# Kernel optimization log

Hardware: AMD Instinct MI355X
Metric: run time of the kernel (lower is better)

Reference implementation:

```python
import jax, jax.numpy as jnp
import numpy as np

B, F, C, NS, P, N = 256, 2048, 16384, 65536, 8, 32
T, W_BU, W_H, P_MARGIN, N_MARGIN = 1.0, 1.0, 10.0, 0.1, 0.1


def setup_inputs() -> dict:
    key = jax.random.key(0)
    ks = jax.random.split(key, 8)
    inputs = jax.random.normal(ks[0], (B, F), jnp.float32)
    targets = jax.random.randint(ks[1], (B,), 0, C)
    # batch global indices: unique (original .item() assumes a single match)
    indexs = jax.random.permutation(ks[2], NS)[:B].astype(jnp.int64) if False else jax.random.permutation(ks[2], jnp.arange(NS))[:B]
    # positive candidates drawn from in-batch indices so they are found in `indexs`
    pos_sel = jax.random.randint(ks[3], (B, P), 0, B)
    ppairs = indexs[pos_sel]
    # negative candidates: arbitrary global indices (mostly not in batch)
    npairs = jax.random.randint(ks[4], (B, N), 0, NS)
    all_label_to_clusterid = jax.random.randint(ks[5], (NS,), 0, C)
    V = jax.random.normal(ks[6], (C, F), jnp.float32)
    V = V / jnp.linalg.norm(V, axis=1, keepdims=True)  # bank rows are L2-normalized by the update rule
    return {"inputs": inputs, "targets": targets, "ppairs": ppairs, "npairs": npairs,
            "indexs": indexs, "all_label_to_clusterid": all_label_to_clusterid, "V": V, "epoch": 1}


def _forward(inputs, targets, ppairs, npairs, indexs, all_label_to_clusterid, V, epoch):
    # Exclusive branch: logits against the memory bank (V treated as constant)
    outputs = (inputs @ V.T) * T  # [B, C]
    logp = jax.nn.log_softmax(outputs, axis=1)
    bu_loss = -jnp.mean(jnp.take_along_axis(logp, targets[:, None], axis=1))

    # ms_loss (use_prior=True, use_table=True)
    ni = inputs / jnp.linalg.norm(inputs, axis=1, keepdims=True)
    sims = ni @ ni.T          # [B, B]
    tsims = ni @ V.T          # [B, C]

    # positives found in the batch: (ppair == indexs).nonzero()
    mp = ppairs[:, :, None] == indexs[None, None, :]        # [B, P, B]
    found_p = jnp.any(mp, axis=2)
    idx_p = jnp.argmax(mp, axis=2)
    psim_b = jnp.take_along_axis(sims, idx_p, axis=1)       # [B, P]
    mask_pb = found_p & (ppairs >= 0)
    # table positive: tsims[i, target] appended if nonzero
    tp = jnp.take_along_axis(tsims, targets[:, None], axis=1)  # [B, 1]
    mask_tp = tp != 0
    psims = jnp.concatenate([psim_b, tp], axis=1)           # [B, P+1]
    pmask = jnp.concatenate([mask_pb, mask_tp], axis=1)

    # negatives found in the batch
    mn = npairs[:, :, None] == indexs[None, None, :]        # [B, N, B]
    found_n = jnp.any(mn, axis=2)
    idx_n = jnp.argmax(mn, axis=2)
    nsim_b = jnp.take_along_axis(sims, idx_n, axis=1)       # [B, N]
    mask_nb = found_n & (npairs >= 0)
    # table negative appended for EVERY npair (indent level in original): tsims[i, clusterid[npair]]
    ncid = all_label_to_clusterid[jnp.clip(npairs, 0, None)]
    tn = jnp.take_along_axis(tsims, ncid, axis=1)           # [B, N]
    mask_tn = (npairs >= 0) & (tn != 0)
    nsims = jnp.concatenate([nsim_b, tn], axis=1)           # [B, 2N]
    nmask = jnp.concatenate([mask_nb, mask_tn], axis=1)

    # thresholds: max(nsims) or -3 (+p_margin); min(psims) or 3 (-n_margin)
    p_thrd = jnp.where(jnp.any(nmask, 1), jnp.max(jnp.where(nmask, nsims, -jnp.inf), 1), -3.0) + P_MARGIN
    n_thrd = jnp.where(jnp.any(pmask, 1), jnp.min(jnp.where(pmask, psims, jnp.inf), 1), 3.0) - N_MARGIN

    hp = pmask & (psims < p_thrd[:, None])
    hn = nmask & (nsims > n_thrd[:, None]) & (nsims < 0.999999)

    hp_sum = jnp.sum(jnp.where(hp, jnp.exp(-2.0 * (psims - 0.5)), 0.0))
    hn_sum = jnp.sum(jnp.where(hn, jnp.exp(50.0 * (nsims - 0.5)), 0.0))
    hp_loss = jnp.where(jnp.any(hp), 0.5 * jnp.log1p(hp_sum), 0.0)
    hn_loss = jnp.where(jnp.any(hn), (1.0 / 50.0) * jnp.log1p(hn_sum), 0.0)
    # original builds hpsims/hnsims with torch.tensor(...), which DETACHES them
    h_loss = jax.lax.stop_gradient(hp_loss + hn_loss)

    loss = W_BU * bu_loss + W_H * h_loss
    return loss, outputs


def reference(inputs, targets, ppairs, npairs, indexs, all_label_to_clusterid, V, epoch):
    return _forward(inputs, targets, ppairs, npairs, indexs, all_label_to_clusterid, V, epoch)
```

## Files before the change

### kernel.cpp

```cpp
#include <hip/hip_runtime.h>
#include <hip/hip_bf16.h>
#include <math.h>

#define B_SZ 256
#define F_SZ 2048
#define C_SZ 16384
#define P_SZ 8
#define N_SZ 32
#define NTILE 256

typedef __bf16 bf16x8 __attribute__((ext_vector_type(8)));
typedef float f32x4 __attribute__((ext_vector_type(4)));
typedef unsigned short us8 __attribute__((ext_vector_type(8)));

typedef __attribute__((address_space(3))) unsigned int lds_u32;
typedef __attribute__((address_space(1))) const unsigned int glb_u32;

#define WAITCNT_VM4   0x0F74
#define WAITCNT_VM0   0x0F70
#define WAITCNT_LGKM0 0xC07F

__device__ __forceinline__ unsigned short f2bf(float x) {
    union { float f; unsigned int u; } v; v.f = x;
    unsigned int r = v.u + 0x7FFFu + ((v.u >> 16) & 1u);
    return (unsigned short)(r >> 16);
}

__global__ __launch_bounds__(256) void prep_kernel(const float* __restrict__ inputs,
                                                   unsigned short* __restrict__ Abf,
                                                   float* __restrict__ norms) {
    const int row = blockIdx.x;
    const int tid = threadIdx.x;
    const float* rp = inputs + (size_t)row * F_SZ + tid * 8;
    float4 v0 = *(const float4*)(rp);
    float4 v1 = *(const float4*)(rp + 4);
    us8 o;
    o[0]=f2bf(v0.x); o[1]=f2bf(v0.y); o[2]=f2bf(v0.z); o[3]=f2bf(v0.w);
    o[4]=f2bf(v1.x); o[5]=f2bf(v1.y); o[6]=f2bf(v1.z); o[7]=f2bf(v1.w);
    *(us8*)(Abf + (size_t)row * F_SZ + tid * 8) = o;
    float ss = v0.x*v0.x + v0.y*v0.y + v0.z*v0.z + v0.w*v0.w
             + v1.x*v1.x + v1.y*v1.y + v1.z*v1.z + v1.w*v1.w;
    __shared__ float red[256];
    red[tid] = ss; __syncthreads();
    for (int s = 128; s > 0; s >>= 1) { if (tid < s) red[tid] += red[tid+s]; __syncthreads(); }
    if (tid == 0) norms[row] = sqrtf(red[0]);
}

#define BM 128
#define BN 64
#define BK 64
#define BPAD 72
#define KITERS (F_SZ / BK)

__global__ __launch_bounds__(256, 2) void gemm_kernel(const unsigned short* __restrict__ Abf,
                                                      const float* __restrict__ V,
                                                      float* __restrict__ Cout,
                                                      float* __restrict__ pmax,
                                                      float* __restrict__ psum) {
    __shared__ unsigned short As[3][BM * BK];
    __shared__ unsigned short Bs[2][BN * BPAD];
    __shared__ float sm[BM * 2], ss2[BM * 2];

    const int tid = threadIdx.x;
    const int lane = tid & 63;
    const int wid = tid >> 6;
    const int wm = wid >> 1, wn = wid & 1;
    const int q = lane >> 4, l16 = lane & 15;

    const int bid = blockIdx.x;
    const int mhalf = (bid >> 3) & 1;
    const int slab  = (bid & 7) | ((bid >> 4) << 3);
    const int bm0 = mhalf * BM;
    const int bn0 = slab * BN;

    f32x4 acc[4][2];
    #pragma unroll
    for (int i = 0; i < 4; i++)
        #pragma unroll
        for (int j = 0; j < 2; j++) acc[i][j] = (f32x4){0.f, 0.f, 0.f, 0.f};

    const int arow = tid >> 3;
    const int akc = (tid & 7) ^ (arow & 7);
    const unsigned short* AgBase = Abf + (size_t)(bm0 + arow) * F_SZ + akc * 8;

    const int bcol = tid >> 2, bseg = tid & 3;
    const float* BgBase = V + (size_t)(bn0 + bcol) * F_SZ + bseg * 16;
    const int bsoff = bcol * BPAD + bseg * 16;

    float4 b0, b1, b2, b3;

    auto issueA = [&](int ring, int k0) {
        #pragma unroll
        for (int j = 0; j < 4; ++j) {
            __builtin_amdgcn_global_load_lds(
                (glb_u32*)(AgBase + (size_t)j * 32 * F_SZ + k0),
                (lds_u32*)&As[ring][(j * 256 + wid * 64) * 8],
                16, 0, 0);
        }
    };
    auto loadB = [&](int k0) {
        b0 = *(const float4*)(BgBase + k0);
        b1 = *(const float4*)(BgBase + k0 + 4);
        b2 = *(const float4*)(BgBase + k0 + 8);
        b3 = *(const float4*)(BgBase + k0 + 12);
    };
    auto writeB = [&](int buf) {
        us8 w0, w1;
        w0[0]=f2bf(b0.x); w0[1]=f2bf(b0.y); w0[2]=f2bf(b0.z); w0[3]=f2bf(b0.w);
        w0[4]=f2bf(b1.x); w0[5]=f2bf(b1.y); w0[6]=f2bf(b1.z); w0[7]=f2bf(b1.w);
        w1[0]=f2bf(b2.x); w1[1]=f2bf(b2.y); w1[2]=f2bf(b2.z); w1[3]=f2bf(b2.w);
        w1[4]=f2bf(b3.x); w1[5]=f2bf(b3.y); w1[6]=f2bf(b3.z); w1[7]=f2bf(b3.w);
        *(us8*)&Bs[buf][bsoff] = w0;
        *(us8*)&Bs[buf][bsoff + 8] = w1;
    };
    auto compute = [&](int ring, int buf) {
        #pragma unroll
        for (int ks = 0; ks < 2; ++ks) {
            bf16x8 af[4], bfv[2];
            const int kc = ks * 4 + q;
            #pragma unroll
            for (int mi = 0; mi < 4; ++mi) {
                const int row = wm * 64 + mi * 16 + l16;
                af[mi] = *(const bf16x8*)&As[ring][row * 64 + (kc ^ (row & 7)) * 8];
            }
            #pragma unroll
            for (int ni = 0; ni < 2; ++ni) {
                const int col = wn * 32 + ni * 16 + l16;
                bfv[ni] = *(const bf16x8*)&Bs[buf][col * BPAD + ks * 32 + q * 8];
            }
            #pragma unroll
            for (int mi = 0; mi < 4; ++mi)
                #pragma unroll
                for (int ni = 0; ni < 2; ++ni)
                    acc[mi][ni] = __builtin_amdgcn_mfma_f32_16x16x32_bf16(af[mi], bfv[ni], acc[mi][ni], 0, 0, 0);
        }
    };

    issueA(0, 0);
    issueA(1, BK);
    loadB(0);
    __builtin_amdgcn_s_waitcnt(WAITCNT_VM0);
    writeB(0);
    __syncthreads();

    int cur = 0;
    int nxt2 = 2;
    #pragma unroll 1
    for (int it = 0; it < KITERS; ++it) {
        if (it + 1 < KITERS) loadB((it + 1) * BK);
        if (it + 2 < KITERS) issueA(nxt2, (it + 2) * BK);
        compute(cur, it & 1);
        if (it + 2 < KITERS)      __builtin_amdgcn_s_waitcnt(WAITCNT_VM4);
        else if (it + 1 < KITERS) __builtin_amdgcn_s_waitcnt(WAITCNT_VM0);
        if (it + 1 < KITERS) {
            writeB((it + 1) & 1);
            __builtin_amdgcn_s_waitcnt(WAITCNT_LGKM0);
            __builtin_amdgcn_s_barrier();
        }
        cur  = (cur == 2) ? 0 : cur + 1;
        nxt2 = (nxt2 == 2) ? 0 : nxt2 + 1;
    }

    #pragma unroll
    for (int mi = 0; mi < 4; ++mi) {
        const int r0 = bm0 + wm * 64 + mi * 16 + q * 4;
        #pragma unroll
        for (int ni = 0; ni < 2; ++ni) {
            const int c0 = bn0 + wn * 32 + ni * 16 + l16;
            #pragma unroll
            for (int r = 0; r < 4; ++r)
                Cout[(size_t)(r0 + r) * C_SZ + c0] = acc[mi][ni][r];
        }
    }

    #pragma unroll
    for (int mi = 0; mi < 4; ++mi) {
        #pragma unroll
        for (int r = 0; r < 4; ++r) {
            float mloc = fmaxf(acc[mi][0][r], acc[mi][1][r]);
            #pragma unroll
            for (int off = 1; off < 16; off <<= 1)
                mloc = fmaxf(mloc, __shfl_xor(mloc, off, 64));
            float sloc = __expf(acc[mi][0][r] - mloc) + __expf(acc[mi][1][r] - mloc);
            #pragma unroll
            for (int off = 1; off < 16; off <<= 1)
                sloc += __shfl_xor(sloc, off, 64);
            if (l16 == 0) {
                const int lrow = wm * 64 + mi * 16 + q * 4 + r;
                sm[lrow * 2 + wn] = mloc;
                ss2[lrow * 2 + wn] = sloc;
            }
        }
    }
    __syncthreads();
    if (tid < BM) {
        float m1 = sm[tid * 2], s1 = ss2[tid * 2];
        float m2 = sm[tid * 2 + 1], s2 = ss2[tid * 2 + 1];
        float nm = fmaxf(m1, m2);
        float s = s1 * __expf(m1 - nm) + s2 * __expf(m2 - nm);
        pmax[(bm0 + tid) * NTILE + slab] = nm;
        psum[(bm0 + tid) * NTILE + slab] = s;
    }
}

__global__ __launch_bounds__(256) void softmax_combine_kernel(
    const float* __restrict__ pmax, const float* __restrict__ psum,
    const float* __restrict__ outputs, const int* __restrict__ targets,
    float* __restrict__ bu_part)
{
    const int row = blockIdx.x;
    const int tid = threadIdx.x;
    __shared__ float rm[256], rs[256];
    rm[tid] = pmax[row * NTILE + tid];
    rs[tid] = psum[row * NTILE + tid];
    __syncthreads();
    for (int s = 128; s > 0; s >>= 1) {
        if (tid < s) {
            float a = rm[tid], sa = rs[tid];
            float b = rm[tid + s], sb = rs[tid + s];
            float nn = fmaxf(a, b);
            rs[tid] = sa * __expf(a - nn) + sb * __expf(b - nn);
            rm[tid] = nn;
        }
        __syncthreads();
    }
    if (tid == 0) {
        float logZ = rm[0] + logf(rs[0]);
        bu_part[row] = -(outputs[(size_t)row * C_SZ + targets[row]] - logZ);
    }
}

__global__ __launch_bounds__(256) void pairs_kernel(
    const float* __restrict__ inputs, const int* __restrict__ targets,
    const int* __restrict__ ppairs, const int* __restrict__ npairs,
    const int* __restrict__ indexs, const int* __restrict__ cluster,
    const float* __restrict__ outputs, const float* __restrict__ norms,
    float* __restrict__ hp_part, float* __restrict__ hn_part,
    int* __restrict__ flag_part)
{
    const int i = blockIdx.x;
    const int tid = threadIdx.x;
    __shared__ int idxbuf[B_SZ];
    __shared__ int pj[P_SZ];
    __shared__ int nj[N_SZ];
    __shared__ float simp[P_SZ];
    __shared__ float simn[N_SZ];
    __shared__ float tnv[N_SZ];
    __shared__ float s_tp;

    idxbuf[tid] = indexs[tid];
    __syncthreads();

    const float* row = outputs + (size_t)i * C_SZ;
    const float ni_norm = norms[i];

    if (tid < P_SZ) {
        int pp = ppairs[i * P_SZ + tid];
        int f = -1;
        if (pp >= 0) for (int j = 0; j < B_SZ; j++) if (idxbuf[j] == pp) { f = j; break; }
        pj[tid] = f;
    } else if (tid < P_SZ + N_SZ) {
        int t = tid - P_SZ;
        int np = npairs[i * N_SZ + t];
        int f = -1;
        if (np >= 0) for (int j = 0; j < B_SZ; j++) if (idxbuf[j] == np) { f = j; break; }
        nj[t] = f;
        int cid = cluster[np < 0 ? 0 : np];
        tnv[t] = row[cid] / ni_norm;
    }
    if (tid == P_SZ + N_SZ) s_tp = row[targets[i]] / ni_norm;
    __syncthreads();

    const int lane = tid & 63, wv = tid >> 6;
    for (int qq = wv; qq < P_SZ + N_SZ; qq += 4) {
        int j = (qq < P_SZ) ? pj[qq] : nj[qq - P_SZ];
        float s = 0.f;
        if (j >= 0) {
            const float* xi = inputs + (size_t)i * F_SZ;
            const float* xj = inputs + (size_t)j * F_SZ;
            float d = 0.f;
            for (int k = lane; k < F_SZ; k += 64) d += xi[k] * xj[k];
            for (int off = 32; off > 0; off >>= 1) d += __shfl_down(d, off);
            s = d / (ni_norm * norms[j]);
        }
        if (lane == 0) { if (qq < P_SZ) simp[qq] = s; else simn[qq - P_SZ] = s; }
    }
    __syncthreads();

    if (tid == 0) {
        float psims[P_SZ + 1]; bool pmask[P_SZ + 1];
        for (int p = 0; p < P_SZ; p++) {
            int pp = ppairs[i * P_SZ + p];
            pmask[p] = (pj[p] >= 0) && (pp >= 0);
            psims[p] = simp[p];
        }
        psims[P_SZ] = s_tp; pmask[P_SZ] = (s_tp != 0.0f);

        float nsims[2 * N_SZ]; bool nmask[2 * N_SZ];
        for (int t = 0; t < N_SZ; t++) {
            int np = npairs[i * N_SZ + t];
            nmask[t] = (nj[t] >= 0) && (np >= 0);
            nsims[t] = simn[t];
            nsims[N_SZ + t] = tnv[t];
            nmask[N_SZ + t] = (np >= 0) && (tnv[t] != 0.0f);
        }
        bool anyp = false, anyn = false;
        float maxn = -INFINITY, minp = INFINITY;
        for (int t = 0; t < 2 * N_SZ; t++) if (nmask[t]) { anyn = true; maxn = fmaxf(maxn, nsims[t]); }
        for (int p = 0; p < P_SZ + 1; p++) if (pmask[p]) { anyp = true; minp = fminf(minp, psims[p]); }
        float p_thrd = (anyn ? maxn : -3.0f) + 0.1f;
        float n_thrd = (anyp ? minp : 3.0f) - 0.1f;
        float hps = 0.f, hns = 0.f; int fl = 0;
        for (int p = 0; p < P_SZ + 1; p++)
            if (pmask[p] && psims[p] < p_thrd) { fl |= 1; hps += expf(-2.0f * (psims[p] - 0.5f)); }
        for (int t = 0; t < 2 * N_SZ; t++)
            if (nmask[t] && nsims[t] > n_thrd && nsims[t] < 0.999999f) { fl |= 2; hns += expf(50.0f * (nsims[t] - 0.5f)); }
        hp_part[i] = hps; hn_part[i] = hns; flag_part[i] = fl;
    }
}

__global__ __launch_bounds__(256) void finalize_kernel(
    const float* __restrict__ bu_part, const float* __restrict__ hp_part,
    const float* __restrict__ hn_part, const int* __restrict__ flag_part,
    float* __restrict__ d_out)
{
    __shared__ float r1[256], r2[256], r3[256];
    __shared__ int rf[256];
    const int tid = threadIdx.x;
    r1[tid] = bu_part[tid]; r2[tid] = hp_part[tid]; r3[tid] = hn_part[tid]; rf[tid] = flag_part[tid];
    __syncthreads();
    for (int s = 128; s > 0; s >>= 1) {
        if (tid < s) { r1[tid] += r1[tid+s]; r2[tid] += r2[tid+s]; r3[tid] += r3[tid+s]; rf[tid] |= rf[tid+s]; }
        __syncthreads();
    }
    if (tid == 0) {
        float bu = r1[0] / (float)B_SZ;
        float hp_loss = (rf[0] & 1) ? 0.5f * log1pf(r2[0]) : 0.0f;
        float hn_loss = (rf[0] & 2) ? (1.0f / 50.0f) * log1pf(r3[0]) : 0.0f;
        d_out[0] = 1.0f * bu + 10.0f * (hp_loss + hn_loss);
    }
}

extern "C" void kernel_launch(void* const* d_in, const int* in_sizes, int n_in,
                              void* d_out, int out_size, void* d_ws, size_t ws_size,
                              hipStream_t stream) {
    const float* inputs  = (const float*)d_in[0];
    const int*   targets = (const int*)d_in[1];
    const int*   ppairs  = (const int*)d_in[2];
    const int*   npairs  = (const int*)d_in[3];
    const int*   indexs  = (const int*)d_in[4];
    const int*   cluster = (const int*)d_in[5];
    const float* V       = (const float*)d_in[6];
    float* out = (float*)d_out;

    char* ws = (char*)d_ws;
    unsigned short* Abf = (unsigned short*)ws;
    float* norms   = (float*)(ws + (size_t)B_SZ * F_SZ * 2);
    float* bu_part = norms + B_SZ;
    float* hp_part = bu_part + B_SZ;
    float* hn_part = hp_part + B_SZ;
    int*   flag_part = (int*)(hn_part + B_SZ);
    float* pmax = (float*)(flag_part + B_SZ);
    float* psum = pmax + (size_t)B_SZ * NTILE;

    prep_kernel<<<B_SZ, 256, 0, stream>>>(inputs, Abf, norms);
    gemm_kernel<<<512, 256, 0, stream>>>(Abf, V, out + 1, pmax, psum);
    softmax_combine_kernel<<<B_SZ, 256, 0, stream>>>(pmax, psum, out + 1, targets, bu_part);
    pairs_kernel<<<B_SZ, 256, 0, stream>>>(inputs, targets, ppairs, npairs, indexs,
                                           cluster, out + 1, norms,
                                           hp_part, hn_part, flag_part);
    finalize_kernel<<<1, 256, 0, stream>>>(bu_part, hp_part, hn_part, flag_part, out);
}
```

Baseline: 300.6 us.

## Deepen B prefetch to two stages, pack bf16 via perm, fuse softmax combine into pairs

The GEMM main loop is unrolled by two and uses two register sets for the fp32 V tiles, so each B tile is loaded two iterations ahead, and the vmcnt wait is relaxed to allow eight loads in flight. The bf16 conversion now packs pairs with a byte-permute instead of per-element round-to-nearest-even, which is cheaper but rounds ties away from zero rather than to even. The separate softmax-combine kernel is merged into the pairs kernel, removing one launch. The extra registers may reduce occupancy.

Result: no change. 301.9 us (+0.4%).

```diff
diff --git a/kernel.cpp b/kernel.cpp
--- a/kernel.cpp
+++ b/kernel.cpp
@@ -16,7 +16,7 @@
 typedef __attribute__((address_space(3))) unsigned int lds_u32;
 typedef __attribute__((address_space(1))) const unsigned int glb_u32;
 
-#define WAITCNT_VM4   0x0F74
+#define WAITCNT_VM8   0x0F78
 #define WAITCNT_VM0   0x0F70
 #define WAITCNT_LGKM0 0xC07F
 
@@ -24,6 +24,11 @@
     union { float f; unsigned int u; } v; v.f = x;
     unsigned int r = v.u + 0x7FFFu + ((v.u >> 16) & 1u);
     return (unsigned short)(r >> 16);
+}
+
+__device__ __forceinline__ unsigned int pk2bf(float x, float y) {
+    union { float f; unsigned int u; } a, b; a.f = x; b.f = y;
+    return __builtin_amdgcn_perm(b.u + 0x8000u, a.u + 0x8000u, 0x07060302u);
 }
 
 __global__ __launch_bounds__(256) void prep_kernel(const float* __restrict__ inputs,
@@ -87,7 +92,8 @@
     const float* BgBase = V + (size_t)(bn0 + bcol) * F_SZ + bseg * 16;
     const int bsoff = bcol * BPAD + bseg * 16;
 
-    float4 b0, b1, b2, b3;
+    float4 a0, a1, a2, a3;
+    float4 c0, c1, c2, c3;
 
     auto issueA = [&](int ring, int k0) {
         #pragma unroll
@@ -98,20 +104,20 @@
                 16, 0, 0);
         }
     };
-    auto loadB = [&](int k0) {
-        b0 = *(const float4*)(BgBase + k0);
-        b1 = *(const float4*)(BgBase + k0 + 4);
-        b2 = *(const float4*)(BgBase + k0 + 8);
-        b3 = *(const float4*)(BgBase + k0 + 12);
-    };
-    auto writeB = [&](int buf) {
-        us8 w0, w1;
-        w0[0]=f2bf(b0.x); w0[1]=f2bf(b0.y); w0[2]=f2bf(b0.z); w0[3]=f2bf(b0.w);
-        w0[4]=f2bf(b1.x); w0[5]=f2bf(b1.y); w0[6]=f2bf(b1.z); w0[7]=f2bf(b1.w);
-        w1[0]=f2bf(b2.x); w1[1]=f2bf(b2.y); w1[2]=f2bf(b2.z); w1[3]=f2bf(b2.w);
-        w1[4]=f2bf(b3.x); w1[5]=f2bf(b3.y); w1[6]=f2bf(b3.z); w1[7]=f2bf(b3.w);
-        *(us8*)&Bs[buf][bsoff] = w0;
-        *(us8*)&Bs[buf][bsoff + 8] = w1;
+    auto loadB0 = [&](int k0) {
+        a0 = *(const float4*)(BgBase + k0);     a1 = *(const float4*)(BgBase + k0 + 4);
+        a2 = *(const float4*)(BgBase + k0 + 8); a3 = *(const float4*)(BgBase + k0 + 12);
+    };
+    auto loadB1 = [&](int k0) {
+        c0 = *(const float4*)(BgBase + k0);     c1 = *(const float4*)(BgBase + k0 + 4);
+        c2 = *(const float4*)(BgBase + k0 + 8); c3 = *(const float4*)(BgBase + k0 + 12);
+    };
+    auto writeB = [&](int buf, int set) {
+        float4 x0 = set ? c0 : a0, x1 = set ? c1 : a1, x2 = set ? c2 : a2, x3 = set ? c3 : a3;
+        uint4 w0 = { pk2bf(x0.x, x0.y), pk2bf(x0.z, x0.w), pk2bf(x1.x, x1.y), pk2bf(x1.z, x1.w) };
+        uint4 w1 = { pk2bf(x2.x, x2.y), pk2bf(x2.z, x2.w), pk2bf(x3.x, x3.y), pk2bf(x3.z, x3.w) };
+        *(uint4*)&Bs[buf][bsoff] = w0;
+        *(uint4*)&Bs[buf][bsoff + 8] = w1;
     };
     auto compute = [&](int ring, int buf) {
         #pragma unroll
@@ -138,27 +144,40 @@
 
     issueA(0, 0);
     issueA(1, BK);
-    loadB(0);
+    loadB0(0);
     __builtin_amdgcn_s_waitcnt(WAITCNT_VM0);
-    writeB(0);
+    writeB(0, 0);
+    loadB1(BK);
     __syncthreads();
 
     int cur = 0;
-    int nxt2 = 2;
     #pragma unroll 1
-    for (int it = 0; it < KITERS; ++it) {
-        if (it + 1 < KITERS) loadB((it + 1) * BK);
-        if (it + 2 < KITERS) issueA(nxt2, (it + 2) * BK);
-        compute(cur, it & 1);
-        if (it + 2 < KITERS)      __builtin_amdgcn_s_waitcnt(WAITCNT_VM4);
-        else if (it + 1 < KITERS) __builtin_amdgcn_s_waitcnt(WAITCNT_VM0);
-        if (it + 1 < KITERS) {
-            writeB((it + 1) & 1);
-            __builtin_amdgcn_s_waitcnt(WAITCNT_LGKM0);
-            __builtin_amdgcn_s_barrier();
-        }
-        cur  = (cur == 2) ? 0 : cur + 1;
-        nxt2 = (nxt2 == 2) ? 0 : nxt2 + 1;
+    for (int it2 = 0; it2 < KITERS; it2 += 2) {
+        {
+            const int it = it2;
+            if (it + 2 < KITERS) { loadB0((it + 2) * BK); issueA((cur + 2) % 3, (it + 2) * BK); }
+            compute(cur, 0);
+            if (it + 2 < KITERS)      __builtin_amdgcn_s_waitcnt(WAITCNT_VM8);
+            else if (it + 1 < KITERS) __builtin_amdgcn_s_waitcnt(WAITCNT_VM0);
+            if (it + 1 < KITERS) {
+                writeB(1, 1);
+                __builtin_amdgcn_s_waitcnt(WAITCNT_LGKM0);
+                __builtin_amdgcn_s_barrier();
+            }
+        }
+        {
+            const int it = it2 + 1;
+            if (it + 2 < KITERS) { loadB1((it + 2) * BK); issueA(cur, (it + 2) * BK); }
+            compute((cur + 1) % 3, 1);
+            if (it + 2 < KITERS)      __builtin_amdgcn_s_waitcnt(WAITCNT_VM8);
+            else if (it + 1 < KITERS) __builtin_amdgcn_s_waitcnt(WAITCNT_VM0);
+            if (it + 1 < KITERS) {
+                writeB(0, 0);
+                __builtin_amdgcn_s_waitcnt(WAITCNT_LGKM0);
+                __builtin_amdgcn_s_barrier();
+            }
+        }
+        cur = (cur + 2) % 3;
     }
 
     #pragma unroll
@@ -166,10 +185,10 @@
         const int r0 = bm0 + wm * 64 + mi * 16 + q * 4;
         #pragma unroll
         for (int ni = 0; ni < 2; ++ni) {
-            const int c0 = bn0 + wn * 32 + ni * 16 + l16;
+            const int c0g = bn0 + wn * 32 + ni * 16 + l16;
             #pragma unroll
             for (int r = 0; r < 4; ++r)
-                Cout[(size_t)(r0 + r) * C_SZ + c0] = acc[mi][ni][r];
+                Cout[(size_t)(r0 + r) * C_SZ + c0g] = acc[mi][ni][r];
         }
     }
 
@@ -203,40 +222,14 @@
     }
 }
 
-__global__ __launch_bounds__(256) void softmax_combine_kernel(
-    const float* __restrict__ pmax, const float* __restrict__ psum,
-    const float* __restrict__ outputs, const int* __restrict__ targets,
-    float* __restrict__ bu_part)
-{
-    const int row = blockIdx.x;
-    const int tid = threadIdx.x;
-    __shared__ float rm[256], rs[256];
-    rm[tid] = pmax[row * NTILE + tid];
-    rs[tid] = psum[row * NTILE + tid];
-    __syncthreads();
-    for (int s = 128; s > 0; s >>= 1) {
-        if (tid < s) {
-            float a = rm[tid], sa = rs[tid];
-            float b = rm[tid + s], sb = rs[tid + s];
-            float nn = fmaxf(a, b);
-            rs[tid] = sa * __expf(a - nn) + sb * __expf(b - nn);
-            rm[tid] = nn;
-        }
-        __syncthreads();
-    }
-    if (tid == 0) {
-        float logZ = rm[0] + logf(rs[0]);
-        bu_part[row] = -(outputs[(size_t)row * C_SZ + targets[row]] - logZ);
-    }
-}
-
 __global__ __launch_bounds__(256) void pairs_kernel(
     const float* __restrict__ inputs, const int* __restrict__ targets,
     const int* __restrict__ ppairs, const int* __restrict__ npairs,
     const int* __restrict__ indexs, const int* __restrict__ cluster,
     const float* __restrict__ outputs, const float* __restrict__ norms,
-    float* __restrict__ hp_part, float* __restrict__ hn_part,
-    int* __restrict__ flag_part)
+    const float* __restrict__ pmax, const float* __restrict__ psum,
+    float* __restrict__ bu_part, float* __restrict__ hp_part,
+    float* __restrict__ hn_part, int* __restrict__ flag_part)
 {
     const int i = blockIdx.x;
     const int tid = threadIdx.x;
@@ -247,12 +240,30 @@
     __shared__ float simn[N_SZ];
     __shared__ float tnv[N_SZ];
     __shared__ float s_tp;
+    __shared__ float rm[256], rs[256];
 
     idxbuf[tid] = indexs[tid];
-    __syncthreads();
+    rm[tid] = pmax[i * NTILE + tid];
+    rs[tid] = psum[i * NTILE + tid];
+    __syncthreads();
+    for (int s = 128; s > 0; s >>= 1) {
+        if (tid < s) {
+            float a = rm[tid], sa = rs[tid];
+            float b = rm[tid + s], sb = rs[tid + s];
+            float nn = fmaxf(a, b);
+            rs[tid] = sa * __expf(a - nn) + sb * __expf(b - nn);
+            rm[tid] = nn;
+        }
+        __syncthreads();
+    }
 
     const float* row = outputs + (size_t)i * C_SZ;
     const float ni_norm = norms[i];
+
+    if (tid == 0) {
+        float logZ = rm[0] + logf(rs[0]);
+        bu_part[i] = -(row[targets[i]] - logZ);
+    }
 
     if (tid < P_SZ) {
         int pp = ppairs[i * P_SZ + tid];
@@ -365,9 +376,8 @@
 
     prep_kernel<<<B_SZ, 256, 0, stream>>>(inputs, Abf, norms);
     gemm_kernel<<<512, 256, 0, stream>>>(Abf, V, out + 1, pmax, psum);
-    softmax_combine_kernel<<<B_SZ, 256, 0, stream>>>(pmax, psum, out + 1, targets, bu_part);
     pairs_kernel<<<B_SZ, 256, 0, stream>>>(inputs, targets, ppairs, npairs, indexs,
-                                           cluster, out + 1, norms,
-                                           hp_part, hn_part, flag_part);
+                                           cluster, out + 1, norms, pmax, psum,
+                                           bu_part, hp_part, hn_part, flag_part);
     finalize_kernel<<<1, 256, 0, stream>>>(bu_part, hp_part, hn_part, flag_part, out);
 }
```
